# Performance work log

Measured on AMD Instinct MI355X. Metric: run time of the kernel, lower is better.

The kernel has to match this reference:

```python
import math
import jax, jax.numpy as jnp
import numpy as np

D_MODEL = 256
N_HEADS = 4
HEAD_DIM = D_MODEL // N_HEADS
MAX_REL = 30


def _rel_pos_encodings(t, d_model):
    # sinusoidal table over clipped relative distances -> [t, t, d_model]
    n = 2 * MAX_REL + 1
    positions = jnp.arange(n, dtype=jnp.float32)[:, None]
    div_term = jnp.exp(jnp.arange(0, d_model, 2, dtype=jnp.float32) * (-math.log(10000.0) / d_model))
    ang = positions * div_term                      # [n, d/2]
    enc = jnp.stack([jnp.sin(ang), jnp.cos(ang)], axis=-1).reshape(n, d_model)
    rng = jnp.arange(t)
    final_mat = jnp.clip(rng[None, :] - rng[:, None], -MAX_REL, MAX_REL) + MAX_REL  # [t, t]
    return enc[final_mat]                           # [t, t, d_model]


def setup_inputs() -> dict:
    key = jax.random.key(0)
    ks = jax.random.split(key, 12)
    d = D_MODEL
    s = 1.0 / math.sqrt(d)
    inp = {
        "inputs": jax.random.normal(ks[0], (16, 512, d), dtype=jnp.float32),
        "ln_gamma": jnp.ones((d,), jnp.float32),
        "ln_beta": jnp.zeros((d,), jnp.float32),
        "Wq": jax.random.normal(ks[1], (d, d), jnp.float32) * s,
        "bq": jnp.zeros((d,), jnp.float32),
        "Wk": jax.random.normal(ks[2], (d, d), jnp.float32) * s,
        "bk": jnp.zeros((d,), jnp.float32),
        "Wv": jax.random.normal(ks[3], (d, d), jnp.float32) * s,
        "bv": jnp.zeros((d,), jnp.float32),
        "Wpos": jax.random.normal(ks[4], (d, d), jnp.float32) * s,
        "bpos": jnp.zeros((d,), jnp.float32),
        "Wo": jax.random.normal(ks[5], (d, d), jnp.float32) * s,
        "bo": jnp.zeros((d,), jnp.float32),
        "u_bias": jax.random.normal(ks[6], (1, N_HEADS, 1, HEAD_DIM), jnp.float32) * 0.02,
        "v_bias": jax.random.normal(ks[7], (1, N_HEADS, 1, HEAD_DIM), jnp.float32) * 0.02,
    }
    return inp


def reference(inputs, ln_gamma, ln_beta, Wq, bq, Wk, bk, Wv, bv, Wpos, bpos, Wo, bo, u_bias, v_bias):
    b, t, d = inputs.shape
    h, hd = N_HEADS, HEAD_DIM
    # LayerNorm (eps=1e-5, torch default)
    mu = jnp.mean(inputs, axis=-1, keepdims=True)
    var = jnp.mean(jnp.square(inputs - mu), axis=-1, keepdims=True)
    x = (inputs - mu) * jax.lax.rsqrt(var + 1e-5) * ln_gamma + ln_beta

    def split_heads(y):
        return y.reshape(b, t, h, hd).transpose(0, 2, 1, 3)  # b h t d

    q = split_heads(x @ Wq.T + bq)
    k = split_heads(x @ Wk.T + bk)
    v = split_heads(x @ Wv.T + bv)

    rel = jax.lax.stop_gradient(_rel_pos_encodings(t, d))    # [t, t, d]
    pos = (rel @ Wpos.T + bpos).reshape(t, t, h, hd)         # [t1, t2, h, hd]

    qk_score = jnp.einsum('bhtd,bhsd->bhts', q + u_bias, k)
    pos_score = jnp.einsum('bhtd,tshd->bhts', q + v_bias, pos)
    scores = (qk_score + pos_score) / math.sqrt(hd)
    attn = jax.nn.softmax(scores, axis=-1)
    ctx = jnp.einsum('bhts,bhsd->bhtd', attn, v)
    ctx = ctx.transpose(0, 2, 1, 3).reshape(b, t, d)
    return ctx @ Wo.T + bo
```

## Files before the change

### kernel.cpp

```cpp
#include <hip/hip_runtime.h>
#include <hip/hip_bf16.h>
#include <math.h>

#define B 16
#define T 512
#define D 256
#define H 4
#define HD 64
#define MAXREL 30
#define NREL 61
#define M_ROWS (B*T)
#define QBLK 64

typedef __attribute__((ext_vector_type(8))) short bf16x8;
typedef __attribute__((ext_vector_type(4))) float f32x4;
typedef unsigned short ush;

__device__ inline ush f2b(float f) {
    __hip_bfloat16 h = __float2bfloat16(f);
    union { __hip_bfloat16 h; ush u; } c; c.h = h; return c.u;
}
__device__ inline float b2f(ush u) {
    union { ush u; __hip_bfloat16 h; } c; c.u = u; return __bfloat162float(c.h);
}
__device__ inline unsigned int pk2(float a, float b) {
    __hip_bfloat162 h = __float22bfloat162_rn(make_float2(a, b));
    union { __hip_bfloat162 h; unsigned int u; } c; c.h = h; return c.u;
}
__device__ inline int swz(int row, int byteoff) {
    return row * 128 + (byteoff ^ ((row & 7) << 4));
}
__device__ inline int swz256(int row, int byteoff) {
    return row * 256 + (byteoff ^ ((row & 7) << 4));
}
__device__ inline int swz512(int row, int byteoff) {
    return row * 512 + (byteoff ^ ((row & 7) << 4));
}

#define SCL 0.1803368801111204f

__global__ __launch_bounds__(256) void prep_kernel(const float* __restrict__ x,
                                                   const float* __restrict__ gamma,
                                                   const float* __restrict__ beta,
                                                   ush* __restrict__ xb,
                                                   const float* __restrict__ Wq, const float* __restrict__ Wk,
                                                   const float* __restrict__ Wv, const float* __restrict__ Wo,
                                                   ush* __restrict__ wb,
                                                   const float* __restrict__ Wpos,
                                                   const float* __restrict__ bpos,
                                                   ush* __restrict__ pospb) {
    __shared__ __attribute__((aligned(16))) ush wpS[64 * 256];
    int bid = blockIdx.x;
    int tid = threadIdx.x;
    if (bid < 2048) {
        int row = bid * 4 + (tid >> 6);
        int lane = tid & 63;
        const float* xr = x + (size_t)row * D;
        float4 v = *(const float4*)(xr + lane * 4);
        float s = v.x + v.y + v.z + v.w;
        #pragma unroll
        for (int off = 32; off; off >>= 1) s += __shfl_xor(s, off);
        float mu = s * (1.f / 256.f);
        float dx = v.x - mu, dy = v.y - mu, dz = v.z - mu, dw = v.w - mu;
        float vs = dx*dx + dy*dy + dz*dz + dw*dw;
        #pragma unroll
        for (int off = 32; off; off >>= 1) vs += __shfl_xor(vs, off);
        float rstd = rsqrtf(vs * (1.f / 256.f) + 1e-5f);
        float4 g = *(const float4*)(gamma + lane * 4);
        float4 bb = *(const float4*)(beta + lane * 4);
        ushort4 o;
        o.x = f2b(dx * rstd * g.x + bb.x);
        o.y = f2b(dy * rstd * g.y + bb.y);
        o.z = f2b(dz * rstd * g.z + bb.z);
        o.w = f2b(dw * rstd * g.w + bb.w);
        *(ushort4*)(xb + (size_t)row * D + lane * 4) = o;
    } else if (bid < 2048 + 256) {
        int b2 = bid - 2048;
        int z = b2 >> 6, xblk = b2 & 63;
        const float* src = z == 0 ? Wq : z == 1 ? Wk : z == 2 ? Wv : Wo;
        int idx = (xblk * 256 + tid) * 4;
        float4 v = *(const float4*)(src + idx);
        ushort4 o;
        o.x = f2b(v.x); o.y = f2b(v.y); o.z = f2b(v.z); o.w = f2b(v.w);
        *(ushort4*)(wb + (size_t)z * 65536 + idx) = o;
    } else {
        int h = bid - 2304;
        int w = tid >> 6, l = tid & 63, lg = l >> 4, ln = l & 15;
        const float* wsrc = Wpos + (size_t)(h * 64) * D;
        #pragma unroll
        for (int c = 0; c < 16; ++c) {
            int idx = c * 256 + tid;
            int row = idx >> 6, col = (idx & 63) * 4;
            float4 v = *(const float4*)(wsrc + (size_t)row * D + col);
            ushort4 o; o.x = f2b(v.x); o.y = f2b(v.y); o.z = f2b(v.z); o.w = f2b(v.w);
            *(ushort4*)((char*)wpS + swz512(row, col * 2)) = o;
        }
        int p = w * 16 + ln;
        bf16x8 af[8];
        #pragma unroll
        for (int ks = 0; ks < 8; ++ks) {
            #pragma unroll
            for (int j = 0; j < 8; ++j) {
                int k = ks * 32 + lg * 8 + j;
                int i = k >> 1;
                float dt = __expf(-(2.f * i) * (9.210340371976184f / 256.f));
                float ang = (float)p * dt;
                float v = (k & 1) ? __cosf(ang) : __sinf(ang);
                af[ks][j] = (short)f2b(v);
            }
        }
        __syncthreads();
        f32x4 acc[4] = {};
        #pragma unroll
        for (int ks = 0; ks < 8; ++ks) {
            int kbyte = (ks * 32 + lg * 8) * 2;
            #pragma unroll
            for (int ct = 0; ct < 4; ++ct) {
                bf16x8 bf = *(const bf16x8*)((const char*)wpS + swz512(ct * 16 + ln, kbyte));
                acc[ct] = __builtin_amdgcn_mfma_f32_16x16x32_bf16(af[ks], bf, acc[ct], 0, 0, 0);
            }
        }
        #pragma unroll
        for (int ct = 0; ct < 4; ++ct) {
            int dcol = ct * 16 + ln;
            float bb = bpos[h * 64 + dcol];
            #pragma unroll
            for (int r = 0; r < 4; ++r) {
                int pr = w * 16 + lg * 4 + r;
                pospb[(size_t)h * 4096 + pr * 64 + dcol] = f2b(acc[ct][r] + bb);
            }
        }
    }
}

__global__ __launch_bounds__(256, 3) void qkv_mfma(const ush* __restrict__ A,
                                                   const ush* __restrict__ wball,
                                                   const float* __restrict__ bq,
                                                   const float* __restrict__ bk,
                                                   const float* __restrict__ bv,
                                                   ush* __restrict__ qb,
                                                   ush* __restrict__ kbuf,
                                                   ush* __restrict__ vtb) {
    __shared__ __attribute__((aligned(16))) ush A_s[128 * 128];
    __shared__ __attribute__((aligned(16))) ush B_s[64 * 128];
    int tid = threadIdx.x;
    int w = tid >> 6, l = tid & 63;
    int lg = l >> 4, ln = l & 15;
    int wr = w >> 1, wc = w & 1;
    int i0 = blockIdx.x * 128;
    int j0 = blockIdx.y * 64;
    int z = blockIdx.z;
    const ush* Wp = wball + (size_t)z * 65536 + (size_t)j0 * D;
    const ush* Ap = A + (size_t)i0 * D;
    const float* bias = z == 0 ? bq : (z == 1 ? bk : bv);
    f32x4 acc[2][4] = {};

    #pragma unroll 1
    for (int kb2 = 0; kb2 < 2; ++kb2) {
        int k0 = kb2 * 128;
        if (kb2) __syncthreads();
        #pragma unroll
        for (int c = 0; c < 8; ++c) {
            int u = c * 256 + tid;
            int row = u >> 4, sub = u & 15;
            *(bf16x8*)((char*)A_s + swz256(row, sub * 16)) = *(const bf16x8*)(Ap + (size_t)row * D + k0 + sub * 8);
        }
        #pragma unroll
        for (int c = 0; c < 4; ++c) {
            int u = c * 256 + tid;
            int row = u >> 4, sub = u & 15;
            *(bf16x8*)((char*)B_s + swz256(row, sub * 16)) = *(const bf16x8*)(Wp + (size_t)row * D + k0 + sub * 8);
        }
        __syncthreads();
        __builtin_amdgcn_s_setprio(1);
        #pragma unroll
        for (int ksub = 0; ksub < 4; ++ksub) {
            int kbyte = ksub * 64 + lg * 16;
            bf16x8 af[2], bfr[4];
            #pragma unroll
            for (int mi = 0; mi < 2; ++mi)
                af[mi] = *(const bf16x8*)((const char*)B_s + swz256(wr * 32 + mi * 16 + ln, kbyte));
            #pragma unroll
            for (int ni = 0; ni < 4; ++ni)
                bfr[ni] = *(const bf16x8*)((const char*)A_s + swz256(wc * 64 + ni * 16 + ln, kbyte));
            #pragma unroll
            for (int mi = 0; mi < 2; ++mi)
                #pragma unroll
                for (int ni = 0; ni < 4; ++ni)
                    acc[mi][ni] = __builtin_amdgcn_mfma_f32_16x16x32_bf16(af[mi], bfr[ni], acc[mi][ni], 0, 0, 0);
        }
        __builtin_amdgcn_s_setprio(0);
    }

    if (z == 2) {
        #pragma unroll
        for (int mi = 0; mi < 2; ++mi) {
            int jb = j0 + wr * 32 + mi * 16 + lg * 4;
            float4 bv4 = *(const float4*)(bias + jb);
            float bvv[4] = {bv4.x, bv4.y, bv4.z, bv4.w};
            #pragma unroll
            for (int ni = 0; ni < 4; ++ni) {
                int t = i0 + wc * 64 + ni * 16 + ln;
                #pragma unroll
                for (int r = 0; r < 4; ++r)
                    vtb[(size_t)(jb + r) * M_ROWS + t] = f2b(acc[mi][ni][r] + bvv[r]);
            }
        }
    } else {
        ush* ob = (z == 0) ? qb : kbuf;
        #pragma unroll
        for (int mi = 0; mi < 2; ++mi) {
            int jb = j0 + wr * 32 + mi * 16 + lg * 4;
            float4 bv4 = *(const float4*)(bias + jb);
            #pragma unroll
            for (int ni = 0; ni < 4; ++ni) {
                int t = i0 + wc * 64 + ni * 16 + ln;
                ushort4 o;
                o.x = f2b(acc[mi][ni][0] + bv4.x); o.y = f2b(acc[mi][ni][1] + bv4.y);
                o.z = f2b(acc[mi][ni][2] + bv4.z); o.w = f2b(acc[mi][ni][3] + bv4.w);
                *(ushort4*)(ob + (size_t)t * D + jb) = o;
            }
        }
    }
}

__global__ __launch_bounds__(256, 2) void outproj_mfma(const ush* __restrict__ A,
                                                       const ush* __restrict__ W,
                                                       const float* __restrict__ bias,
                                                       float* __restrict__ of) {
    __shared__ __attribute__((aligned(16))) ush A_s[64 * 128];
    __shared__ __attribute__((aligned(16))) ush B_s[64 * 128];
    int tid = threadIdx.x;
    int w = tid >> 6, l = tid & 63;
    int lg = l >> 4, ln = l & 15;
    int wr = w >> 1, wc = w & 1;
    int i0 = blockIdx.x * 64;
    int j0 = blockIdx.y * 64;
    const ush* Ap = A + (size_t)i0 * D;
    const ush* Wp = W + (size_t)j0 * D;
    f32x4 acc[2][2] = {};

    #pragma unroll 1
    for (int kb2 = 0; kb2 < 2; ++kb2) {
        int k0 = kb2 * 128;
        if (kb2) __syncthreads();
        #pragma unroll
        for (int c = 0; c < 4; ++c) {
            int u = c * 256 + tid;
            int row = u >> 4, sub = u & 15;
            *(bf16x8*)((char*)A_s + swz256(row, sub * 16)) = *(const bf16x8*)(Ap + (size_t)row * D + k0 + sub * 8);
            *(bf16x8*)((char*)B_s + swz256(row, sub * 16)) = *(const bf16x8*)(Wp + (size_t)row * D + k0 + sub * 8);
        }
        __syncthreads();
        __builtin_amdgcn_s_setprio(1);
        #pragma unroll
        for (int ksub = 0; ksub < 4; ++ksub) {
            int kbyte = ksub * 64 + lg * 16;
            bf16x8 af[2], bfr[2];
            #pragma unroll
            for (int mi = 0; mi < 2; ++mi)
                af[mi] = *(const bf16x8*)((const char*)B_s + swz256(wr * 32 + mi * 16 + ln, kbyte));
            #pragma unroll
            for (int ni = 0; ni < 2; ++ni)
                bfr[ni] = *(const bf16x8*)((const char*)A_s + swz256(wc * 32 + ni * 16 + ln, kbyte));
            #pragma unroll
            for (int mi = 0; mi < 2; ++mi)
                #pragma unroll
                for (int ni = 0; ni < 2; ++ni)
                    acc[mi][ni] = __builtin_amdgcn_mfma_f32_16x16x32_bf16(af[mi], bfr[ni], acc[mi][ni], 0, 0, 0);
        }
        __builtin_amdgcn_s_setprio(0);
    }

    #pragma unroll
    for (int mi = 0; mi < 2; ++mi) {
        int jb = j0 + wr * 32 + mi * 16 + lg * 4;
        float4 bv4 = *(const float4*)(bias + jb);
        #pragma unroll
        for (int ni = 0; ni < 2; ++ni) {
            int t = i0 + wc * 32 + ni * 16 + ln;
            float4 o;
            o.x = acc[mi][ni][0] + bv4.x; o.y = acc[mi][ni][1] + bv4.y;
            o.z = acc[mi][ni][2] + bv4.z; o.w = acc[mi][ni][3] + bv4.w;
            *(float4*)(of + (size_t)t * D + jb) = o;
        }
    }
}

__global__ __launch_bounds__(256, 3) void attn_mfma(const ush* __restrict__ qb,
                                                    const ush* __restrict__ kb,
                                                    const ush* __restrict__ vtb,
                                                    const ush* __restrict__ pospb,
                                                    const float* __restrict__ u_bias,
                                                    const float* __restrict__ v_bias,
                                                    ush* __restrict__ ctxb) {
    __shared__ __attribute__((aligned(16))) ush Kd[2][64 * 64];
    __shared__ __attribute__((aligned(16))) ush Vd[2][64 * 64];
    __shared__ __attribute__((aligned(16))) ush pdS[4][16 * 66];
    __shared__ __attribute__((aligned(16))) ush PlS[4][16 * 64];

    int tid = threadIdx.x;
    int w = tid >> 6;
    int l = tid & 63;
    int lg = l >> 4, ln = l & 15;
    int bh = blockIdx.x;
    int b = bh >> 2, h = bh & 3;
    int t0 = blockIdx.y * QBLK;
    const size_t baseBH = ((size_t)b * T) * D + h * HD;

    bf16x8 qu[2], qv[2];
    {
        const ush* qrow = qb + baseBH + (size_t)(t0 + w * 16 + ln) * D;
        int c0 = lg * 8;
        #pragma unroll
        for (int ks = 0; ks < 2; ++ks) {
            bf16x8 ld = *(const bf16x8*)(qrow + ks * 32 + c0);
            float4 ub0 = *(const float4*)(u_bias + h * HD + ks * 32 + c0);
            float4 ub1 = *(const float4*)(u_bias + h * HD + ks * 32 + c0 + 4);
            float4 vb0 = *(const float4*)(v_bias + h * HD + ks * 32 + c0);
            float4 vb1 = *(const float4*)(v_bias + h * HD + ks * 32 + c0 + 4);
            float ubv[8] = {ub0.x,ub0.y,ub0.z,ub0.w,ub1.x,ub1.y,ub1.z,ub1.w};
            float vbv[8] = {vb0.x,vb0.y,vb0.z,vb0.w,vb1.x,vb1.y,vb1.z,vb1.w};
            #pragma unroll
            for (int j = 0; j < 8; ++j) {
                float f = b2f((ush)ld[j]);
                qu[ks][j] = (short)f2b((f + ubv[j]) * SCL);
                qv[ks][j] = (short)f2b((f + vbv[j]) * SCL);
            }
        }
    }

    int r0 = tid >> 3,          c0 = tid & 7;
    int r1 = (tid + 256) >> 3,  c1 = (tid + 256) & 7;
    const ush* kbase = kb + baseBH;
    const ush* vbase = vtb + (size_t)(h * HD) * M_ROWS + (size_t)b * T;
    const ush* pbase = pospb + (size_t)h * 4096;

    {
        bf16x8 pp0 = *(const bf16x8*)(pbase + r0 * 64 + c0 * 8);
        bf16x8 pp1 = *(const bf16x8*)(pbase + r1 * 64 + c1 * 8);
        bf16x8 k0 = *(const bf16x8*)(kbase + (size_t)r0 * D + c0 * 8);
        bf16x8 k1 = *(const bf16x8*)(kbase + (size_t)r1 * D + c1 * 8);
        bf16x8 v0 = *(const bf16x8*)(vbase + (size_t)r0 * M_ROWS + c0 * 8);
        bf16x8 v1 = *(const bf16x8*)(vbase + (size_t)r1 * M_ROWS + c1 * 8);
        *(bf16x8*)((char*)Kd[1] + swz(r0, c0 * 16)) = pp0;
        *(bf16x8*)((char*)Kd[1] + swz(r1, c1 * 16)) = pp1;
        *(bf16x8*)((char*)Kd[0] + swz(r0, c0 * 16)) = k0;
        *(bf16x8*)((char*)Kd[0] + swz(r1, c1 * 16)) = k1;
        *(bf16x8*)((char*)Vd[0] + swz(r0, c0 * 16)) = v0;
        *(bf16x8*)((char*)Vd[0] + swz(r1, c1 * 16)) = v1;
    }
    bf16x8 sk0 = *(const bf16x8*)(kbase + (size_t)(64 + r0) * D + c0 * 8);
    bf16x8 sk1 = *(const bf16x8*)(kbase + (size_t)(64 + r1) * D + c1 * 8);
    bf16x8 sv0 = *(const bf16x8*)(vbase + (size_t)r0 * M_ROWS + 64 + c0 * 8);
    bf16x8 sv1 = *(const bf16x8*)(vbase + (size_t)r1 * M_ROWS + 64 + c1 * 8);
    __syncthreads();

    ush* pdW = pdS[w];
    {
        f32x4 pacc[4] = {};
        #pragma unroll
        for (int ks = 0; ks < 2; ++ks)
            #pragma unroll
            for (int ct = 0; ct < 4; ++ct) {
                bf16x8 bf = *(const bf16x8*)((const char*)Kd[1] + swz(ct * 16 + ln, (ks * 32 + lg * 8) * 2));
                pacc[ct] = __builtin_amdgcn_mfma_f32_16x16x32_bf16(qv[ks], bf, pacc[ct], 0, 0, 0);
            }
        #pragma unroll
        for (int ct = 0; ct < 4; ++ct)
            #pragma unroll
            for (int r = 0; r < 4; ++r)
                pdW[(lg * 4 + r) * 66 + ct * 16 + ln] = f2b(pacc[ct][r]);
    }
    float pdlo = b2f(pdW[ln * 66 + 0]);
    float pdhi = b2f(pdW[ln * 66 + 60]);
    __syncthreads();

    f32x4 lacc = {};
    f32x4 o_acc[4] = {};
    ush* pw = PlS[w];
    bf16x8 ones;
    #pragma unroll
    for (int j = 0; j < 8; ++j) ones[j] = (short)0x3F80;
    int cur = 0;

    for (int st = 0; st < 8; ++st) {
        int s0 = st * 64;
        if (st < 7) {
            char* kdst = (char*)Kd[cur ^ 1];
            char* vdst = (char*)Vd[cur ^ 1];
            *(bf16x8*)(kdst + swz(r0, c0 * 16)) = sk0;
            *(bf16x8*)(kdst + swz(r1, c1 * 16)) = sk1;
            *(bf16x8*)(vdst + swz(r0, c0 * 16)) = sv0;
            *(bf16x8*)(vdst + swz(r1, c1 * 16)) = sv1;
        }
        if (st < 6) {
            int sn = s0 + 128;
            sk0 = *(const bf16x8*)(kbase + (size_t)(sn + r0) * D + c0 * 8);
            sk1 = *(const bf16x8*)(kbase + (size_t)(sn + r1) * D + c1 * 8);
            sv0 = *(const bf16x8*)(vbase + (size_t)r0 * M_ROWS + sn + c0 * 8);
            sv1 = *(const bf16x8*)(vbase + (size_t)r1 * M_ROWS + sn + c1 * 8);
        }

        const char* Kc = (const char*)Kd[cur];
        const char* Vc = (const char*)Vd[cur];

        int dlt = s0 - t0;
        float cinit = (dlt >= 128) ? pdhi : ((dlt <= -128) ? pdlo : 0.f);
        f32x4 sacc[4];
        #pragma unroll
        for (int ct = 0; ct < 4; ++ct)
            #pragma unroll
            for (int r = 0; r < 4; ++r) sacc[ct][r] = cinit;

        __builtin_amdgcn_s_setprio(1);
        #pragma unroll
        for (int ks = 0; ks < 2; ++ks)
            #pragma unroll
            for (int ct = 0; ct < 4; ++ct) {
                bf16x8 kf = *(const bf16x8*)(Kc + swz(ct * 16 + ln, (ks * 32 + lg * 8) * 2));
                sacc[ct] = __builtin_amdgcn_mfma_f32_16x16x32_bf16(kf, qu[ks], sacc[ct], 0, 0, 0);
            }
        __builtin_amdgcn_s_setprio(0);

        if (dlt > -128 && dlt < 128) {
            int t_glob = t0 + w * 16 + ln;
            #pragma unroll
            for (int ct = 0; ct < 4; ++ct) {
                #pragma unroll
                for (int r = 0; r < 4; ++r) {
                    int s_g = s0 + ct * 16 + lg * 4 + r;
                    int rel = s_g - t_glob;
                    rel = rel < -MAXREL ? -MAXREL : (rel > MAXREL ? MAXREL : rel);
                    sacc[ct][r] += b2f(pdW[ln * 66 + rel + MAXREL]);
                }
            }
        }

        #pragma unroll
        for (int ct = 0; ct < 4; ++ct)
            #pragma unroll
            for (int r = 0; r < 4; ++r)
                sacc[ct][r] = exp2f(sacc[ct][r]);

        #pragma unroll
        for (int ct = 0; ct < 4; ++ct)
            #pragma unroll
            for (int rr = 0; rr < 2; ++rr)
                *(unsigned int*)((char*)pw + swz(ln, (ct * 16 + lg * 4 + rr * 2) * 2)) =
                    pk2(sacc[ct][rr * 2], sacc[ct][rr * 2 + 1]);

        __builtin_amdgcn_s_setprio(1);
        #pragma unroll
        for (int ks = 0; ks < 2; ++ks) {
            bf16x8 pa = *(const bf16x8*)((const char*)pw + swz(ln, (ks * 32 + lg * 8) * 2));
            #pragma unroll
            for (int cd = 0; cd < 4; ++cd) {
                bf16x8 bv8 = *(const bf16x8*)(Vc + swz(cd * 16 + ln, (ks * 32 + lg * 8) * 2));
                o_acc[cd] = __builtin_amdgcn_mfma_f32_16x16x32_bf16(pa, bv8, o_acc[cd], 0, 0, 0);
            }
            lacc = __builtin_amdgcn_mfma_f32_16x16x32_bf16(pa, ones, lacc, 0, 0, 0);
        }
        __builtin_amdgcn_s_setprio(0);

        __syncthreads();
        cur ^= 1;
    }

    float inv[4];
    #pragma unroll
    for (int r = 0; r < 4; ++r) inv[r] = 1.f / lacc[r];
    #pragma unroll
    for (int cd = 0; cd < 4; ++cd)
        #pragma unroll
        for (int r = 0; r < 4; ++r) {
            int t_loc = w * 16 + lg * 4 + r;
            ctxb[baseBH + (size_t)(t0 + t_loc) * D + cd * 16 + ln] = f2b(o_acc[cd][r] * inv[r]);
        }
}

extern "C" void kernel_launch(void* const* d_in, const int* in_sizes, int n_in,
                              void* d_out, int out_size, void* d_ws, size_t ws_size,
                              hipStream_t stream) {
    const float* inputs  = (const float*)d_in[0];
    const float* ln_g    = (const float*)d_in[1];
    const float* ln_b    = (const float*)d_in[2];
    const float* Wq      = (const float*)d_in[3];
    const float* bq      = (const float*)d_in[4];
    const float* Wk      = (const float*)d_in[5];
    const float* bk      = (const float*)d_in[6];
    const float* Wv      = (const float*)d_in[7];
    const float* bv      = (const float*)d_in[8];
    const float* Wpos    = (const float*)d_in[9];
    const float* bpos    = (const float*)d_in[10];
    const float* Wo      = (const float*)d_in[11];
    const float* bo      = (const float*)d_in[12];
    const float* u_bias  = (const float*)d_in[13];
    const float* v_bias  = (const float*)d_in[14];
    float* out = (float*)d_out;

    char* w = (char*)d_ws;
    ush* xb    = (ush*)w;  w += (size_t)M_ROWS * D * 2;
    ush* qb    = (ush*)w;  w += (size_t)M_ROWS * D * 2;
    ush* kbuf  = (ush*)w;  w += (size_t)M_ROWS * D * 2;
    ush* vtb   = (ush*)w;  w += (size_t)M_ROWS * D * 2;
    ush* ctxb  = (ush*)w;  w += (size_t)M_ROWS * D * 2;
    ush* wb    = (ush*)w;  w += (size_t)4 * 65536 * 2;
    ush* pospb = (ush*)w;  w += (size_t)4 * 64 * 64 * 2;

    prep_kernel<<<2048 + 256 + 4, 256, 0, stream>>>(inputs, ln_g, ln_b, xb,
                                                    Wq, Wk, Wv, Wo, wb,
                                                    Wpos, bpos, pospb);

    qkv_mfma<<<dim3(M_ROWS / 128, 4, 3), 256, 0, stream>>>(xb, wb, bq, bk, bv, qb, kbuf, vtb);

    attn_mfma<<<dim3(B * H, T / QBLK), 256, 0, stream>>>(qb, kbuf, vtb, pospb, u_bias, v_bias, ctxb);

    outproj_mfma<<<dim3(M_ROWS / 64, 4), 256, 0, stream>>>(ctxb, wb + 3 * 65536, bo, out);
}
```

Baseline: 42.51 us.

## Double attention query block to 128 with 512-thread blocks sharing K/V tiles

The attention kernel now processes 128 query rows per block using 8 waves, so each staged K/V tile in shared memory is reused by twice as many query rows. Each thread loads one chunk instead of two, and the relative-position window bounds are widened to cover the larger query span. The LayerNorm prep path also processes 16 rows per block instead of 4, reducing block count. The grid halves to 256 attention blocks, which lowers parallelism and occupancy slack in exchange for less K/V reload traffic.

```diff
diff --git a/kernel.cpp b/kernel.cpp
--- a/kernel.cpp
+++ b/kernel.cpp
@@ -10,7 +10,7 @@
 #define MAXREL 30
 #define NREL 61
 #define M_ROWS (B*T)
-#define QBLK 64
+#define QBLK 128
 
 typedef __attribute__((ext_vector_type(8))) short bf16x8;
 typedef __attribute__((ext_vector_type(4))) float f32x4;
@@ -52,30 +52,33 @@
     __shared__ __attribute__((aligned(16))) ush wpS[64 * 256];
     int bid = blockIdx.x;
     int tid = threadIdx.x;
-    if (bid < 2048) {
-        int row = bid * 4 + (tid >> 6);
+    if (bid < 512) {
         int lane = tid & 63;
-        const float* xr = x + (size_t)row * D;
-        float4 v = *(const float4*)(xr + lane * 4);
-        float s = v.x + v.y + v.z + v.w;
-        #pragma unroll
-        for (int off = 32; off; off >>= 1) s += __shfl_xor(s, off);
-        float mu = s * (1.f / 256.f);
-        float dx = v.x - mu, dy = v.y - mu, dz = v.z - mu, dw = v.w - mu;
-        float vs = dx*dx + dy*dy + dz*dz + dw*dw;
-        #pragma unroll
-        for (int off = 32; off; off >>= 1) vs += __shfl_xor(vs, off);
-        float rstd = rsqrtf(vs * (1.f / 256.f) + 1e-5f);
         float4 g = *(const float4*)(gamma + lane * 4);
         float4 bb = *(const float4*)(beta + lane * 4);
-        ushort4 o;
-        o.x = f2b(dx * rstd * g.x + bb.x);
-        o.y = f2b(dy * rstd * g.y + bb.y);
-        o.z = f2b(dz * rstd * g.z + bb.z);
-        o.w = f2b(dw * rstd * g.w + bb.w);
-        *(ushort4*)(xb + (size_t)row * D + lane * 4) = o;
-    } else if (bid < 2048 + 256) {
-        int b2 = bid - 2048;
+        #pragma unroll
+        for (int it = 0; it < 4; ++it) {
+            int row = bid * 16 + it * 4 + (tid >> 6);
+            const float* xr = x + (size_t)row * D;
+            float4 v = *(const float4*)(xr + lane * 4);
+            float s = v.x + v.y + v.z + v.w;
+            #pragma unroll
+            for (int off = 32; off; off >>= 1) s += __shfl_xor(s, off);
+            float mu = s * (1.f / 256.f);
+            float dx = v.x - mu, dy = v.y - mu, dz = v.z - mu, dw = v.w - mu;
+            float vs = dx*dx + dy*dy + dz*dz + dw*dw;
+            #pragma unroll
+            for (int off = 32; off; off >>= 1) vs += __shfl_xor(vs, off);
+            float rstd = rsqrtf(vs * (1.f / 256.f) + 1e-5f);
+            ushort4 o;
+            o.x = f2b(dx * rstd * g.x + bb.x);
+            o.y = f2b(dy * rstd * g.y + bb.y);
+            o.z = f2b(dz * rstd * g.z + bb.z);
+            o.w = f2b(dw * rstd * g.w + bb.w);
+            *(ushort4*)(xb + (size_t)row * D + lane * 4) = o;
+        }
+    } else if (bid < 512 + 256) {
+        int b2 = bid - 512;
         int z = b2 >> 6, xblk = b2 & 63;
         const float* src = z == 0 ? Wq : z == 1 ? Wk : z == 2 ? Wv : Wo;
         int idx = (xblk * 256 + tid) * 4;
@@ -84,7 +87,7 @@
         o.x = f2b(v.x); o.y = f2b(v.y); o.z = f2b(v.z); o.w = f2b(v.w);
         *(ushort4*)(wb + (size_t)z * 65536 + idx) = o;
     } else {
-        int h = bid - 2304;
+        int h = bid - 768;
         int w = tid >> 6, l = tid & 63, lg = l >> 4, ln = l & 15;
         const float* wsrc = Wpos + (size_t)(h * 64) * D;
         #pragma unroll
@@ -287,7 +290,7 @@
     }
 }
 
-__global__ __launch_bounds__(256, 3) void attn_mfma(const ush* __restrict__ qb,
+__global__ __launch_bounds__(512, 2) void attn_mfma(const ush* __restrict__ qb,
                                                     const ush* __restrict__ kb,
                                                     const ush* __restrict__ vtb,
                                                     const ush* __restrict__ pospb,
@@ -296,8 +299,8 @@
                                                     ush* __restrict__ ctxb) {
     __shared__ __attribute__((aligned(16))) ush Kd[2][64 * 64];
     __shared__ __attribute__((aligned(16))) ush Vd[2][64 * 64];
-    __shared__ __attribute__((aligned(16))) ush pdS[4][16 * 66];
-    __shared__ __attribute__((aligned(16))) ush PlS[4][16 * 64];
+    __shared__ __attribute__((aligned(16))) ush pdS[8][16 * 66];
+    __shared__ __attribute__((aligned(16))) ush PlS[8][16 * 64];
 
     int tid = threadIdx.x;
     int w = tid >> 6;
@@ -330,30 +333,21 @@
         }
     }
 
-    int r0 = tid >> 3,          c0 = tid & 7;
-    int r1 = (tid + 256) >> 3,  c1 = (tid + 256) & 7;
+    int r0 = tid >> 3, c0 = tid & 7;
     const ush* kbase = kb + baseBH;
     const ush* vbase = vtb + (size_t)(h * HD) * M_ROWS + (size_t)b * T;
     const ush* pbase = pospb + (size_t)h * 4096;
 
     {
         bf16x8 pp0 = *(const bf16x8*)(pbase + r0 * 64 + c0 * 8);
-        bf16x8 pp1 = *(const bf16x8*)(pbase + r1 * 64 + c1 * 8);
         bf16x8 k0 = *(const bf16x8*)(kbase + (size_t)r0 * D + c0 * 8);
-        bf16x8 k1 = *(const bf16x8*)(kbase + (size_t)r1 * D + c1 * 8);
         bf16x8 v0 = *(const bf16x8*)(vbase + (size_t)r0 * M_ROWS + c0 * 8);
-        bf16x8 v1 = *(const bf16x8*)(vbase + (size_t)r1 * M_ROWS + c1 * 8);
         *(bf16x8*)((char*)Kd[1] + swz(r0, c0 * 16)) = pp0;
-        *(bf16x8*)((char*)Kd[1] + swz(r1, c1 * 16)) = pp1;
         *(bf16x8*)((char*)Kd[0] + swz(r0, c0 * 16)) = k0;
-        *(bf16x8*)((char*)Kd[0] + swz(r1, c1 * 16)) = k1;
         *(bf16x8*)((char*)Vd[0] + swz(r0, c0 * 16)) = v0;
-        *(bf16x8*)((char*)Vd[0] + swz(r1, c1 * 16)) = v1;
     }
     bf16x8 sk0 = *(const bf16x8*)(kbase + (size_t)(64 + r0) * D + c0 * 8);
-    bf16x8 sk1 = *(const bf16x8*)(kbase + (size_t)(64 + r1) * D + c1 * 8);
     bf16x8 sv0 = *(const bf16x8*)(vbase + (size_t)r0 * M_ROWS + 64 + c0 * 8);
-    bf16x8 sv1 = *(const bf16x8*)(vbase + (size_t)r1 * M_ROWS + 64 + c1 * 8);
     __syncthreads();
 
     ush* pdW = pdS[w];
@@ -387,27 +381,26 @@
     for (int st = 0; st < 8; ++st) {
         int s0 = st * 64;
         if (st < 7) {
-            char* kdst = (char*)Kd[cur ^ 1];
-            char* vdst = (char*)Vd[cur ^ 1];
-            *(bf16x8*)(kdst + swz(r0, c0 * 16)) = sk0;
-            *(bf16x8*)(kdst + swz(r1, c1 * 16)) = sk1;
-            *(bf16x8*)(vdst + swz(r0, c0 * 16)) = sv0;
-            *(bf16x8*)(vdst + swz(r1, c1 * 16)) = sv1;
+            *(bf16x8*)((char*)Kd[cur ^ 1] + swz(r0, c0 * 16)) = sk0;
+            *(bf16x8*)((char*)Vd[cur ^ 1] + swz(r0, c0 * 16)) = sv0;
         }
         if (st < 6) {
             int sn = s0 + 128;
             sk0 = *(const bf16x8*)(kbase + (size_t)(sn + r0) * D + c0 * 8);
-            sk1 = *(const bf16x8*)(kbase + (size_t)(sn + r1) * D + c1 * 8);
             sv0 = *(const bf16x8*)(vbase + (size_t)r0 * M_ROWS + sn + c0 * 8);
-            sv1 = *(const bf16x8*)(vbase + (size_t)r1 * M_ROWS + sn + c1 * 8);
         }
 
         const char* Kc = (const char*)Kd[cur];
         const char* Vc = (const char*)Vd[cur];
 
         int dlt = s0 - t0;
-        float cinit = (dlt >= 128) ? pdhi : ((dlt <= -128) ? pdlo : 0.f);
+        int below = dlt <= -(QBLK + MAXREL + 33);
+        (void)below;
+        float cinit;
         f32x4 sacc[4];
+        if (dlt >= 192) cinit = pdhi;
+        else if (dlt <= -128) cinit = pdlo;
+        else cinit = 0.f;
         #pragma unroll
         for (int ct = 0; ct < 4; ++ct)
             #pragma unroll
@@ -423,7 +416,7 @@
             }
         __builtin_amdgcn_s_setprio(0);
 
-        if (dlt > -128 && dlt < 128) {
+        if (dlt > -128 && dlt < 192) {
             int t_glob = t0 + w * 16 + ln;
             #pragma unroll
             for (int ct = 0; ct < 4; ++ct) {
@@ -508,13 +501,13 @@
     ush* wb    = (ush*)w;  w += (size_t)4 * 65536 * 2;
     ush* pospb = (ush*)w;  w += (size_t)4 * 64 * 64 * 2;
 
-    prep_kernel<<<2048 + 256 + 4, 256, 0, stream>>>(inputs, ln_g, ln_b, xb,
-                                                    Wq, Wk, Wv, Wo, wb,
-                                                    Wpos, bpos, pospb);
+    prep_kernel<<<512 + 256 + 4, 256, 0, stream>>>(inputs, ln_g, ln_b, xb,
+                                                   Wq, Wk, Wv, Wo, wb,
+                                                   Wpos, bpos, pospb);
 
     qkv_mfma<<<dim3(M_ROWS / 128, 4, 3), 256, 0, stream>>>(xb, wb, bq, bk, bv, qb, kbuf, vtb);
 
-    attn_mfma<<<dim3(B * H, T / QBLK), 256, 0, stream>>>(qb, kbuf, vtb, pospb, u_bias, v_bias, ctxb);
+    attn_mfma<<<dim3(B * H, T / QBLK), 512, 0, stream>>>(qb, kbuf, vtb, pospb, u_bias, v_bias, ctxb);
 
     outproj_mfma<<<dim3(M_ROWS / 64, 4), 256, 0, stream>>>(ctxb, wb + 3 * 65536, bo, out);
 }
```

Result: faster. 41.19 us (-3.1%).
